# Kernel tuning notes

Measured on AMD Instinct MI355X. Metric: run time of the kernel, lower is better.

## Reference

```python
import jax, jax.numpy as jnp
import numpy as np

B, L, D = 32, 256, 1024
ALIGN = 1024
FF = 2048
NUM_CLASSES = 3


def setup_inputs() -> dict:
    key = jax.random.key(0)
    ks = jax.random.split(key, 10)
    u = lambda k, shape: jax.random.uniform(k, shape, jnp.float32, -1.0, 1.0)
    return {
        "premises": jax.random.normal(ks[0], (B, L, D), jnp.float32),
        "hypotheses": jax.random.normal(ks[1], (B, L, D), jnp.float32),
        "W_F": u(ks[2], (D, ALIGN)),
        "W_G": u(ks[3], (2 * D, FF)),
        "W1": u(ks[4], (2 * FF, FF)) * 0.02,
        "b1": jnp.zeros((FF,), jnp.float32),
        "W2": u(ks[5], (FF, FF)) * 0.02,
        "b2": jnp.zeros((FF,), jnp.float32),
        "W3": u(ks[6], (FF, NUM_CLASSES)) * 0.02,
        "b3": jnp.zeros((NUM_CLASSES,), jnp.float32),
    }


def reference(premises, hypotheses, W_F, W_G, W1, b1, W2, b2, W3, b3):
    # ---- align: tanh-projected cross attention ----
    F_p = jnp.tanh(jnp.einsum("bpd,da->bpa", premises, W_F))      # [B,Lp,A]
    F_h = jnp.tanh(jnp.einsum("bhd,da->bha", hypotheses, W_F))    # [B,Lh,A]
    eijs = jnp.einsum("bpa,bha->bph", F_p, F_h)                   # [B,Lp,Lh]
    attn = jax.nn.softmax(eijs, axis=-1)                          # tf.nn.softmax: last axis
    betas = jnp.einsum("bph,bhd->bpd", attn, hypotheses)          # [B,Lp,D]
    alphas = jnp.einsum("bph,bpd->bhd", attn, premises)           # [B,Lh,D]

    # ---- compare (dropout is identity: p_keep = 1.0 at eval) ----
    V1 = jnp.tanh(jnp.concatenate([premises, betas], axis=2) @ W_G)    # [B,Lp,FF]
    V2 = jnp.tanh(jnp.concatenate([hypotheses, alphas], axis=2) @ W_G) # [B,Lh,FF]

    # ---- aggregate: sum-pool over sequence, concat ----
    agg = jnp.concatenate([V1.sum(axis=1), V2.sum(axis=1)], axis=1)    # [B,2*FF]

    # ---- classifier MLP ----
    a1 = jnp.tanh(agg @ W1 + b1)
    a2 = jnp.tanh(a1 @ W2 + b2)
    logits = a2 @ W3 + b3                                              # [B,3]
    return logits
```

## Files before the change

### kernel.cpp

```cpp
#include <hip/hip_runtime.h>
#include <hip/hip_bf16.h>
#include <stdint.h>


typedef __attribute__((ext_vector_type(8))) short    short8_t;
typedef __attribute__((ext_vector_type(4))) float    float4_t;
typedef __attribute__((ext_vector_type(8))) _Float16 half8_t;
typedef __attribute__((ext_vector_type(4))) _Float16 half4_t;
typedef __attribute__((ext_vector_type(2))) _Float16 half2_t;

#define DEVI static __device__ __forceinline__

DEVI short f2bf(float f) {
  union { float f; unsigned u; } v; v.f = f;
  unsigned r = v.u + 0x7fffu + ((v.u >> 16) & 1u);
  return (short)(r >> 16);
}
DEVI float bf2f(short s) {
  union { unsigned u; float f; } v;
  v.u = ((unsigned)(unsigned short)s) << 16;
  return v.f;
}
DEVI void split2(float x, short& hi, short& lo) {
  hi = f2bf(x);
  lo = f2bf(x - bf2f(hi));
}
DEVI float fast_tanh(float x) {
  float e = __expf(2.0f * x);
  return 1.0f - 2.0f / (e + 1.0f);
}
DEVI void gload16(const void* g, void* l) {
  __builtin_amdgcn_global_load_lds(
      (const __attribute__((address_space(1))) void*)g,
      (__attribute__((address_space(3))) void*)l, 16, 0, 0);
}

template <int DO_TANH, int OUT_MODE>
__global__ __launch_bounds__(256) void gemm_nt_split(
    const short* __restrict__ Ah, const short* __restrict__ Al, int lda, long sA,
    const short* __restrict__ Bh, const short* __restrict__ Bl, int ldb, long sB,
    void* __restrict__ Ch, void* __restrict__ Cl, int ldc, long sC,
    int M, int K, int kslices)
{
  __shared__ __align__(16) short Ash[128 * 32];
  __shared__ __align__(16) short Asl[128 * 32];
  __shared__ __align__(16) short Bsh[128 * 32];
  __shared__ __align__(16) short Bsl[128 * 32];

  const int z  = blockIdx.z;
  const int zb = z / kslices;
  const int Ksub = K / kslices;
  const int zk = z - zb * kslices;
  const int kbeg = zk * Ksub, kend = kbeg + Ksub;

  Ah += (size_t)zb * sA;  Al += (size_t)zb * sA;
  Bh += (size_t)zb * sB;  Bl += (size_t)zb * sB;

  const int row0 = blockIdx.x * 128;
  const int col0 = blockIdx.y * 128;

  const int t    = threadIdx.x;
  const int lane = t & 63;
  const int wave = t >> 6;
  const int wr = wave >> 1, wc = wave & 1;
  const int m15 = lane & 15, q = lane >> 4;

  const int schk = ((t & 3) ^ ((t >> 3) & 3)) * 8;
  const short* pAh = Ah + (size_t)(row0 + (t >> 2)) * lda + kbeg + schk;
  const short* pAl = Al + (size_t)(row0 + (t >> 2)) * lda + kbeg + schk;
  const short* pBh = Bh + (size_t)(col0 + (t >> 2)) * ldb + kbeg + schk;
  const short* pBl = Bl + (size_t)(col0 + (t >> 2)) * ldb + kbeg + schk;
  const size_t a64 = (size_t)64 * lda, b64 = (size_t)64 * ldb;
  short* lAh = &Ash[wave * 512];
  short* lAl = &Asl[wave * 512];
  short* lBh = &Bsh[wave * 512];
  short* lBl = &Bsl[wave * 512];

  const int fs2 = (q ^ ((m15 >> 1) & 3)) * 8;

  float4_t acc[4][4];
#pragma unroll
  for (int i = 0; i < 4; ++i)
#pragma unroll
    for (int j = 0; j < 4; ++j) acc[i][j] = (float4_t)0.0f;

  for (int k0 = kbeg; k0 < kend; k0 += 32) {
    gload16(pAh, lAh);  gload16(pAh + a64, lAh + 2048);
    gload16(pAl, lAl);  gload16(pAl + a64, lAl + 2048);
    gload16(pBh, lBh);  gload16(pBh + b64, lBh + 2048);
    gload16(pBl, lBl);  gload16(pBl + b64, lBl + 2048);
    pAh += 32; pAl += 32; pBh += 32; pBl += 32;
    __syncthreads();

    short8_t ah[4], al[4];
#pragma unroll
    for (int i = 0; i < 4; ++i) {
      const int ra = (wr * 64 + i * 16 + m15) * 32 + fs2;
      ah[i] = *(const short8_t*)&Ash[ra];
      al[i] = *(const short8_t*)&Asl[ra];
    }
#pragma unroll
    for (int j = 0; j < 4; ++j) {
      const int rb = (wc * 64 + j * 16 + m15) * 32 + fs2;
      short8_t bh = *(const short8_t*)&Bsh[rb];
      short8_t bl = *(const short8_t*)&Bsl[rb];
#pragma unroll
      for (int i = 0; i < 4; ++i) {
        acc[i][j] = __builtin_amdgcn_mfma_f32_16x16x32_bf16(ah[i], bh, acc[i][j], 0, 0, 0);
        acc[i][j] = __builtin_amdgcn_mfma_f32_16x16x32_bf16(ah[i], bl, acc[i][j], 0, 0, 0);
        acc[i][j] = __builtin_amdgcn_mfma_f32_16x16x32_bf16(al[i], bh, acc[i][j], 0, 0, 0);
      }
    }
    __syncthreads();
  }

  short* Chs = (short*)Ch + (size_t)zb * sC;
  short* Cls = (short*)Cl + (size_t)zb * sC;
  float* Cf  = (float*)Ch + (size_t)(OUT_MODE == 2 ? z : zb) * sC;
#pragma unroll
  for (int i = 0; i < 4; ++i) {
#pragma unroll
    for (int r = 0; r < 4; ++r) {
      int gm = row0 + wr * 64 + i * 16 + q * 4 + r;
      if (gm < M) {
#pragma unroll
        for (int j = 0; j < 4; ++j) {
          int gn = col0 + wc * 64 + j * 16 + m15;
          float v = acc[i][j][r];
          if (DO_TANH) v = fast_tanh(v);
          if (OUT_MODE == 2) {
            Cf[(size_t)gm * ldc + gn] = v;
          } else {
            short hi, lo; split2(v, hi, lo);
            Chs[(size_t)gm * ldc + gn] = hi;
            Cls[(size_t)gm * ldc + gn] = lo;
          }
        }
      }
    }
  }
}

__global__ __launch_bounds__(256) void gemm_f16(
    const _Float16* __restrict__ A, int lda, long sA,
    const _Float16* __restrict__ B, int ldb, long sB,
    _Float16* __restrict__ C, int ldc, long sC,
    int K, int bxor)
{
  __shared__ __align__(16) _Float16 As[2 * 128 * 32];
  __shared__ __align__(16) _Float16 Bs[2 * 128 * 32];

  const int z = blockIdx.z;
  A += (size_t)z * sA;
  B += (size_t)(z ^ bxor) * sB;

  const int row0 = blockIdx.x * 128;
  const int col0 = blockIdx.y * 128;
  const int t = threadIdx.x, lane = t & 63, wave = t >> 6;
  const int wr = wave >> 1, wc = wave & 1;
  const int m15 = lane & 15, q = lane >> 4;

  const int srow = wave * 32 + (lane >> 2);
  const int cg   = ((lane & 3) ^ ((lane >> 3) & 3)) * 8;
  const _Float16* gA0 = A + (size_t)(row0 + srow) * lda + cg;
  const _Float16* gA1 = gA0 + (size_t)16 * lda;
  const _Float16* gB0 = B + (size_t)(col0 + srow) * ldb + cg;
  const _Float16* gB1 = gB0 + (size_t)16 * ldb;
  const _Float16* gA0b = gA0 + 32;
  const _Float16* gA1b = gA1 + 32;
  const _Float16* gB0b = gB0 + 32;
  const _Float16* gB1b = gB1 + 32;
  _Float16* lA0  = &As[(wave * 32) * 32];
  _Float16* lA1  = &As[(wave * 32 + 16) * 32];
  _Float16* lB0  = &Bs[(wave * 32) * 32];
  _Float16* lB1  = &Bs[(wave * 32 + 16) * 32];
  _Float16* lA0b = lA0 + 4096;
  _Float16* lA1b = lA1 + 4096;
  _Float16* lB0b = lB0 + 4096;
  _Float16* lB1b = lB1 + 4096;

  const int fs = (q ^ ((m15 >> 1) & 3)) * 8;
  int aoff[4], boff[4];
#pragma unroll
  for (int i = 0; i < 4; ++i) {
    aoff[i] = (wr * 64 + i * 16 + m15) * 32 + fs;
    boff[i] = (wc * 64 + i * 16 + m15) * 32 + fs;
  }

  float4_t acc[4][4];
#pragma unroll
  for (int i = 0; i < 4; ++i)
#pragma unroll
    for (int j = 0; j < 4; ++j) acc[i][j] = (float4_t)0.0f;

  for (int k0 = 0; k0 < K; k0 += 64) {
    gload16(gA0, lA0);  gload16(gA1, lA1);
    gload16(gB0, lB0);  gload16(gB1, lB1);
    gload16(gA0b, lA0b); gload16(gA1b, lA1b);
    gload16(gB0b, lB0b); gload16(gB1b, lB1b);
    gA0 += 64; gA1 += 64; gB0 += 64; gB1 += 64;
    gA0b += 64; gA1b += 64; gB0b += 64; gB1b += 64;
    __syncthreads();

#pragma unroll
    for (int h = 0; h < 2; ++h) {
      half8_t af[4], bfr[4];
#pragma unroll
      for (int i = 0; i < 4; ++i) af[i]  = *(const half8_t*)&As[h * 4096 + aoff[i]];
#pragma unroll
      for (int j = 0; j < 4; ++j) bfr[j] = *(const half8_t*)&Bs[h * 4096 + boff[j]];
#pragma unroll
      for (int i = 0; i < 4; ++i)
#pragma unroll
        for (int j = 0; j < 4; ++j)
          acc[i][j] = __builtin_amdgcn_mfma_f32_16x16x32_f16(af[i], bfr[j], acc[i][j], 0, 0, 0);
    }
    __syncthreads();
  }

  {
    _Float16* Cp = C + (size_t)z * sC;
#pragma unroll
    for (int i = 0; i < 4; ++i)
#pragma unroll
      for (int r = 0; r < 4; ++r) {
        int gm = row0 + wr * 64 + i * 16 + q * 4 + r;
#pragma unroll
        for (int j = 0; j < 4; ++j) {
          int gn = col0 + wc * 64 + j * 16 + m15;
          Cp[(size_t)gm * ldc + gn] = (_Float16)acc[i][j][r];
        }
      }
  }
}

__global__ __launch_bounds__(512, 2) void gemm_f16_sum8(
    const _Float16* __restrict__ A, int lda,
    const _Float16* __restrict__ B, int ldb,
    int K, float* __restrict__ agg)
{
  __shared__ __align__(16) _Float16 LDS[4][2 * 256 * 32];

  const int row0 = blockIdx.x * 256;
  const int col0 = blockIdx.y * 256;
  const int tid  = threadIdx.x;
  const int lane = tid & 63, wave = tid >> 6;
  const int wr = wave >> 2, wc = wave & 3;
  const int m15 = lane & 15, q = lane >> 4;
  const int nt = K / 32;

  const int srow = wave * 32 + (lane >> 2);
  const int cg   = ((lane & 3) ^ ((lane >> 3) & 3)) * 8;
  const _Float16* gA = A + (size_t)(row0 + srow) * lda + cg;
  const _Float16* gB = B + (size_t)(col0 + srow) * ldb + cg;

  auto stageA = [&](int t) {
    const _Float16* g = gA + t * 32;
    _Float16* l = &LDS[t & 3][wave * 1024];
    gload16(g, l);
    gload16(g + (size_t)16 * lda, l + 512);
  };
  auto stageB = [&](int t) {
    const _Float16* g = gB + t * 32;
    _Float16* l = &LDS[t & 3][8192 + wave * 1024];
    gload16(g, l);
    gload16(g + (size_t)16 * ldb, l + 512);
  };

  const int xq = (q ^ ((m15 >> 1) & 3)) * 8;
  int aoff[8], boff[4];
#pragma unroll
  for (int i = 0; i < 8; ++i)
    aoff[i] = (wr * 128 + i * 16 + m15) * 32 + xq;
#pragma unroll
  for (int j = 0; j < 4; ++j)
    boff[j] = 8192 + (wc * 64 + j * 16 + m15) * 32 + xq;

  float4_t acc[8][4];
#pragma unroll
  for (int i = 0; i < 8; ++i)
#pragma unroll
    for (int j = 0; j < 4; ++j) acc[i][j] = (float4_t)0.0f;

  stageA(0); stageB(0);
  stageA(1); stageB(1);
  asm volatile("s_waitcnt vmcnt(4)");
  __builtin_amdgcn_s_barrier();

  for (int t = 0; t < nt; ++t) {
    const _Float16* buf = &LDS[t & 3][0];
    __builtin_amdgcn_sched_barrier(0);

    half8_t a0[4], a1[4], bb[4];
#pragma unroll
    for (int i = 0; i < 4; ++i) a0[i] = *(const half8_t*)&buf[aoff[i]];
#pragma unroll
    for (int j = 0; j < 4; ++j) bb[j] = *(const half8_t*)&buf[boff[j]];
#pragma unroll
    for (int i = 0; i < 4; ++i) a1[i] = *(const half8_t*)&buf[aoff[4 + i]];

    if (t + 2 < nt) { stageA(t + 2); stageB(t + 2); }

    __builtin_amdgcn_s_setprio(1);
#pragma unroll
    for (int i = 0; i < 4; ++i)
#pragma unroll
      for (int j = 0; j < 4; ++j)
        acc[i][j] = __builtin_amdgcn_mfma_f32_16x16x32_f16(a0[i], bb[j], acc[i][j], 0, 0, 0);
#pragma unroll
    for (int i = 0; i < 4; ++i)
#pragma unroll
      for (int j = 0; j < 4; ++j)
        acc[4 + i][j] = __builtin_amdgcn_mfma_f32_16x16x32_f16(a1[i], bb[j], acc[4 + i][j], 0, 0, 0);
    __builtin_amdgcn_s_setprio(0);

    __builtin_amdgcn_sched_barrier(0);
    if (t + 2 < nt) {
      asm volatile("s_waitcnt vmcnt(4)");
    } else if (t + 1 < nt) {
      asm volatile("s_waitcnt vmcnt(0)");
    }
    __builtin_amdgcn_s_barrier();
  }

  const int half_ = row0 >= 8192;
  const int b     = (row0 & 8191) >> 8;
#pragma unroll
  for (int j = 0; j < 4; ++j) {
    float s = 0.0f;
#pragma unroll
    for (int i = 0; i < 8; ++i)
#pragma unroll
      for (int r = 0; r < 4; ++r) s += fast_tanh(acc[i][j][r]);
    s += __shfl_xor(s, 16);
    s += __shfl_xor(s, 32);
    if (q == 0) {
      int col = col0 + wc * 64 + j * 16 + m15;
      atomicAdd(&agg[(size_t)b * 4096 + half_ * 2048 + col], s);
    }
  }
}

__global__ __launch_bounds__(256) void transpose_w(
    const float* __restrict__ WF, short* __restrict__ oh, short* __restrict__ ol,
    const float* __restrict__ WG, _Float16* __restrict__ og)
{
  __shared__ float tile[32][33];
  const int id = blockIdx.x;
  const int tx = threadIdx.x & 31, ty = threadIdx.x >> 5;
  if (id < 1024) {
    const int c0 = (id & 31) * 32, r0 = (id >> 5) * 32;
#pragma unroll
    for (int i = 0; i < 4; ++i) {
      int r = ty + i * 8;
      tile[r][tx] = WF[(size_t)(r0 + r) * 1024 + c0 + tx];
    }
    __syncthreads();
#pragma unroll
    for (int i = 0; i < 4; ++i) {
      int cc = ty + i * 8;
      float v = tile[tx][cc];
      short hi, lo; split2(v, hi, lo);
      size_t o = (size_t)(c0 + cc) * 1024 + r0 + tx;
      oh[o] = hi;
      ol[o] = lo;
    }
  } else {
    const int t2 = id - 1024;
    const int c0 = (t2 & 63) * 32, r0 = (t2 >> 6) * 32;
#pragma unroll
    for (int i = 0; i < 4; ++i) {
      int r = ty + i * 8;
      tile[r][tx] = WG[(size_t)(r0 + r) * 2048 + c0 + tx];
    }
    __syncthreads();
#pragma unroll
    for (int i = 0; i < 4; ++i) {
      int cc = ty + i * 8;
      og[(size_t)(c0 + cc) * 2048 + r0 + tx] = (_Float16)tile[tx][cc];
    }
  }
}

__global__ __launch_bounds__(256) void transpose_b2b(
    const short* __restrict__ in, short* __restrict__ out,
    int R, int C, long sIn, long sOut)
{
  __shared__ short tile[32][33];
  in  += (size_t)blockIdx.z * sIn;
  out += (size_t)blockIdx.z * sOut;
  const int tx = threadIdx.x & 31, ty = threadIdx.x >> 5;
  const int c0 = blockIdx.x * 32, r0 = blockIdx.y * 32;
#pragma unroll
  for (int i = 0; i < 4; ++i) {
    int r = ty + i * 8;
    tile[r][tx] = in[(size_t)(r0 + r) * C + c0 + tx];
  }
  __syncthreads();
#pragma unroll
  for (int i = 0; i < 4; ++i) {
    int cc = ty + i * 8;
    out[(size_t)(c0 + cc) * R + r0 + tx] = tile[tx][cc];
  }
}

__global__ __launch_bounds__(256) void conv_in_t(
    const float* __restrict__ P, const float* __restrict__ Hh,
    short* __restrict__ oh, short* __restrict__ ol,
    _Float16* __restrict__ cat, _Float16* __restrict__ phbt,
    float* __restrict__ agg)
{
  __shared__ __align__(16) float tile[64][68];
  const int zb   = blockIdx.z;
  const int half = zb >> 5, b = zb & 31;
  const int bid = (zb * 4 + blockIdx.y) * 16 + blockIdx.x;
  if (bid < 128) {
    float4_t zz = (float4_t)0.0f;
    *(float4_t*)&agg[(size_t)bid * 1024 + threadIdx.x * 4] = zz;
  }
  const float* in = (half ? Hh : P) + (size_t)b * 256 * 1024;
  const int c0 = blockIdx.x * 64;
  const int r0 = blockIdx.y * 64;
  const int t  = threadIdx.x;
  const int rl = t >> 4;
  const int c4 = (t & 15) * 4;
  const size_t rowbase = (size_t)half * 8192 + (size_t)b * 256;
#pragma unroll
  for (int i = 0; i < 4; ++i) {
    int r = rl + i * 16;
    float4 v = *(const float4*)&in[(size_t)(r0 + r) * 1024 + c0 + c4];
    *(float4*)&tile[r][c4] = v;
    short4 h, l;
    split2(v.x, h.x, l.x); split2(v.y, h.y, l.y);
    split2(v.z, h.z, l.z); split2(v.w, h.w, l.w);
    size_t o = (rowbase + r0 + r) * 1024 + c0 + c4;
    *(short4*)&oh[o] = h;
    *(short4*)&ol[o] = l;
    half4_t c16;
    c16.x = (_Float16)v.x; c16.y = (_Float16)v.y;
    c16.z = (_Float16)v.z; c16.w = (_Float16)v.w;
    *(half4_t*)&cat[(rowbase + r0 + r) * 2048 + c0 + c4] = c16;
  }
  __syncthreads();
  _Float16* op = phbt + (size_t)zb * 1024 * 256;
  const int tx = t & 31;
  const int w  = t >> 5;
#pragma unroll
  for (int i = 0; i < 8; ++i) {
    int cc = w + i * 8;
    half2_t p;
    p.x = (_Float16)tile[tx * 2][cc];
    p.y = (_Float16)tile[tx * 2 + 1][cc];
    *(half2_t*)&op[(size_t)(c0 + cc) * 256 + r0 + tx * 2] = p;
  }
}

__global__ __launch_bounds__(256) void softmax_rows(
    const float* __restrict__ e, _Float16* __restrict__ attn)
{
  const int row  = blockIdx.x * 4 + (threadIdx.x >> 6);
  const int lane = threadIdx.x & 63;
  const size_t base = ((size_t)(row >> 8) * 4) * 65536
                    + (size_t)(row & 255) * 256 + lane * 4;
  const float4 v0 = *(const float4*)&e[base];
  const float4 v1 = *(const float4*)&e[base + 65536];
  const float4 v2 = *(const float4*)&e[base + 2 * 65536];
  const float4 v3 = *(const float4*)&e[base + 3 * 65536];
  float4 v;
  v.x = (v0.x + v1.x) + (v2.x + v3.x);
  v.y = (v0.y + v1.y) + (v2.y + v3.y);
  v.z = (v0.z + v1.z) + (v2.z + v3.z);
  v.w = (v0.w + v1.w) + (v2.w + v3.w);
  float m = fmaxf(fmaxf(v.x, v.y), fmaxf(v.z, v.w));
#pragma unroll
  for (int off = 32; off; off >>= 1) m = fmaxf(m, __shfl_xor(m, off));
  float e0 = __expf(v.x - m), e1 = __expf(v.y - m);
  float e2 = __expf(v.z - m), e3 = __expf(v.w - m);
  float s = e0 + e1 + e2 + e3;
#pragma unroll
  for (int off = 32; off; off >>= 1) s += __shfl_xor(s, off);
  float inv = 1.0f / s;
  half4_t o;
  o.x = (_Float16)(e0 * inv); o.y = (_Float16)(e1 * inv);
  o.z = (_Float16)(e2 * inv); o.w = (_Float16)(e3 * inv);
  *(half4_t*)&attn[(size_t)row * 256 + lane * 4] = o;
}

__global__ __launch_bounds__(256) void skinny_gemm(
    const float* __restrict__ A, const float* __restrict__ B,
    float* __restrict__ outp, int N, int K)
{
  __shared__ float Asl[256][33];
  const int n0 = blockIdx.x * 64;
  const int k0 = blockIdx.y * 256;
  const int t  = threadIdx.x;
#pragma unroll
  for (int j = 0; j < 32; ++j) {
    Asl[t][j] = A[(size_t)j * K + k0 + t];
  }
  __syncthreads();
  const int l = t & 63, w = t >> 6;
  const int n = n0 + l;
  float acc[8] = {0.f, 0.f, 0.f, 0.f, 0.f, 0.f, 0.f, 0.f};
  const float* Bp = B + (size_t)k0 * N + n;
#pragma unroll 4
  for (int k = 0; k < 256; ++k) {
    float bv = Bp[(size_t)k * N];
#pragma unroll
    for (int m = 0; m < 8; ++m)
      acc[m] += Asl[k][w * 8 + m] * bv;
  }
  float* o = outp + (size_t)blockIdx.y * 32 * N;
#pragma unroll
  for (int m = 0; m < 8; ++m)
    o[(size_t)(w * 8 + m) * N + n] = acc[m];
}

__global__ __launch_bounds__(256) void bias_sum_tanh(
    const float* __restrict__ parts, int nslice,
    const float* __restrict__ bias, float* __restrict__ o, int n)
{
  int i = blockIdx.x * 256 + threadIdx.x;
  if (i < n) {
    float s = 0.0f;
    for (int sl = 0; sl < nslice; ++sl) s += parts[(size_t)sl * n + i];
    o[i] = fast_tanh(s + bias[i & 2047]);
  }
}

__global__ __launch_bounds__(256) void logits2(
    const float* __restrict__ c2parts, const float* __restrict__ b2,
    const float* __restrict__ W3, const float* __restrict__ b3,
    float* __restrict__ out)
{
  const int b = blockIdx.x, t = threadIdx.x;
  float p0 = 0.f, p1 = 0.f, p2 = 0.f;
  for (int k = t; k < 2048; k += 256) {
    float c = 0.0f;
#pragma unroll
    for (int sl = 0; sl < 8; ++sl) c += c2parts[(size_t)sl * 65536 + b * 2048 + k];
    float a = fast_tanh(c + b2[k]);
    p0 += a * W3[k * 3 + 0];
    p1 += a * W3[k * 3 + 1];
    p2 += a * W3[k * 3 + 2];
  }
#pragma unroll
  for (int off = 32; off; off >>= 1) {
    p0 += __shfl_xor(p0, off);
    p1 += __shfl_xor(p1, off);
    p2 += __shfl_xor(p2, off);
  }
  __shared__ float red[4][3];
  if ((t & 63) == 0) {
    red[t >> 6][0] = p0; red[t >> 6][1] = p1; red[t >> 6][2] = p2;
  }
  __syncthreads();
  if (t < 3) out[b * 3 + t] = b3[t] + red[0][t] + red[1][t] + red[2][t] + red[3][t];
}

extern "C" void kernel_launch(void* const* d_in, const int* in_sizes, int n_in,
                              void* d_out, int out_size, void* d_ws, size_t ws_size,
                              hipStream_t stream) {
  (void)in_sizes; (void)n_in; (void)out_size; (void)ws_size;
  const float* P   = (const float*)d_in[0];
  const float* H   = (const float*)d_in[1];
  const float* W_F = (const float*)d_in[2];
  const float* W_G = (const float*)d_in[3];
  const float* W1  = (const float*)d_in[4];
  const float* b1  = (const float*)d_in[5];
  const float* W2  = (const float*)d_in[6];
  const float* b2  = (const float*)d_in[7];
  const float* W3  = (const float*)d_in[8];
  const float* b3  = (const float*)d_in[9];
  float* out = (float*)d_out;

  char* wsp = (char*)d_ws;
  auto alloc = [&](size_t bytes) {
    char* p = wsp;
    wsp += (bytes + 255) & ~(size_t)255;
    return p;
  };
  short*    Pp_h  = (short*)alloc(16384ull * 1024 * 2);
  short*    Pp_l  = (short*)alloc(16384ull * 1024 * 2);
  _Float16* Cat16 = (_Float16*)alloc(16384ull * 2048 * 2);
  short*    Fbuf  = (short*)alloc(32ull * 1024 * 1024 * 2);
  _Float16* PHbT  = (_Float16*)alloc(64ull * 1024 * 256 * 2);
  short*    WFT_h = (short*)alloc(1024ull * 1024 * 2);
  short*    WFT_l = (short*)alloc(1024ull * 1024 * 2);
  _Float16* WGT16 = (_Float16*)alloc(2048ull * 2048 * 2);
  _Float16* attn  = (_Float16*)alloc(32ull * 256 * 256 * 2);
  _Float16* attnT = (_Float16*)alloc(32ull * 256 * 256 * 2);
  float*    agg   = (float*)alloc(32ull * 4096 * 4);
  float*    a1f   = (float*)alloc(32ull * 2048 * 4);

  short* F_h = Fbuf;
  short* F_l = Fbuf + 16384ull * 1024;
  float* eparts  = (float*)Pp_h;
  float* c1parts = (float*)Pp_l;
  float* c2parts = (float*)(Pp_l + 4ull * 1024 * 1024);

  conv_in_t<<<dim3(16, 4, 64), 256, 0, stream>>>(P, H, Pp_h, Pp_l, Cat16, PHbT, agg);
  transpose_w<<<5120, 256, 0, stream>>>(W_F, WFT_h, WFT_l, W_G, WGT16);

  gemm_nt_split<1, 1><<<dim3(128, 8, 1), 256, 0, stream>>>(
      Pp_h, Pp_l, 1024, 0, WFT_h, WFT_l, 1024, 0,
      F_h, F_l, 1024, 0, 16384, 1024, 1);

  gemm_nt_split<0, 2><<<dim3(2, 2, 128), 256, 0, stream>>>(
      F_h, F_l, 1024, 256 * 1024,
      F_h + 8192ull * 1024, F_l + 8192ull * 1024, 1024, 256 * 1024,
      eparts, nullptr, 256, 65536, 256, 1024, 4);

  softmax_rows<<<2048, 256, 0, stream>>>(eparts, attn);
  transpose_b2b<<<dim3(8, 8, 32), 256, 0, stream>>>(
      (const short*)attn, (short*)attnT, 256, 256, 65536, 65536);

  gemm_f16<<<dim3(2, 8, 64), 256, 0, stream>>>(
      attn, 256, 65536, PHbT, 256, 1024 * 256,
      Cat16 + 1024, 2048, 256 * 2048, 256, 32);

  gemm_f16_sum8<<<dim3(64, 8, 1), 512, 0, stream>>>(
      Cat16, 2048, WGT16, 2048, 2048, agg);

  skinny_gemm<<<dim3(32, 16), 256, 0, stream>>>(agg, W1, c1parts, 2048, 4096);
  bias_sum_tanh<<<256, 256, 0, stream>>>(c1parts, 16, b1, a1f, 32 * 2048);
  skinny_gemm<<<dim3(32, 8), 256, 0, stream>>>(a1f, W2, c2parts, 2048, 2048);
  logits2<<<32, 256, 0, stream>>>(c2parts, b2, W3, b3, out);
}
```

Measured before the change: 560.4 us.

## Add dedicated triple-buffered split-bf16 GEMM for tanh W_F projection

Replaces the generic split-bf16 NT GEMM for the F = tanh(X·W_F) projection with a specialised kernel. It uses 512-thread blocks, 128x256 tiles, a three-slot LDS ring filled by direct global-to-LDS loads two k-steps ahead, XOR-swizzled LDS addressing to avoid bank conflicts, and raised wave priority around the MFMA block. The goal is to hide global load latency and improve MFMA use in the largest GEMM. The cost is 144KB of LDS per block, which limits occupancy, and hard-coded sizes that tie the kernel to these shapes.

```diff
diff --git a/kernel.cpp b/kernel.cpp
--- a/kernel.cpp
+++ b/kernel.cpp
@@ -33,6 +33,121 @@
   __builtin_amdgcn_global_load_lds(
       (const __attribute__((address_space(1))) void*)g,
       (__attribute__((address_space(3))) void*)l, 16, 0, 0);
+}
+
+__global__ __launch_bounds__(512, 2) void gemm_split_f(
+    const short* __restrict__ Ah, const short* __restrict__ Al,
+    const short* __restrict__ Bh, const short* __restrict__ Bl,
+    short* __restrict__ Fh, short* __restrict__ Fl)
+{
+  __shared__ __align__(16) short LDS[3][24576];
+
+  const int id   = blockIdx.x;
+  const int row0 = (id >> 2) * 128;
+  const int col0 = (id & 3) * 256;
+  const int tid  = threadIdx.x;
+  const int lane = tid & 63, wave = tid >> 6;
+  const int wr = wave >> 2, wc = wave & 3;
+  const int m15 = lane & 15, q = lane >> 4;
+  const int nt = 1024 / 32;
+
+  const int cg = ((lane & 3) ^ ((lane >> 3) & 3)) * 8;
+  const short* gptr[6];
+  int ldsoff[6];
+#pragma unroll
+  for (int c = 0; c < 6; ++c) {
+    const int f0 = wave * 96 + c * 16;
+    const int fr = f0 + (lane >> 2);
+    const short* base;
+    size_t roff;
+    if (f0 < 128)      { base = Ah; roff = (size_t)(row0 + fr) * 1024; }
+    else if (f0 < 256) { base = Al; roff = (size_t)(row0 + fr - 128) * 1024; }
+    else if (f0 < 512) { base = Bh; roff = (size_t)(col0 + fr - 256) * 1024; }
+    else               { base = Bl; roff = (size_t)(col0 + fr - 512) * 1024; }
+    gptr[c]   = base + roff + cg;
+    ldsoff[c] = f0 * 32;
+  }
+  auto stage = [&](short* slotbase, int kt) {
+#pragma unroll
+    for (int c = 0; c < 6; ++c)
+      gload16(gptr[c] + kt * 32, slotbase + ldsoff[c]);
+  };
+
+  const int xq = (q ^ ((m15 >> 1) & 3)) * 8;
+  int arow[4], brow[4];
+#pragma unroll
+  for (int i = 0; i < 4; ++i) {
+    arow[i] = (wr * 64 + i * 16 + m15) * 32 + xq;
+    brow[i] = 8192 + (wc * 64 + i * 16 + m15) * 32 + xq;
+  }
+
+  float4_t acc[4][4];
+#pragma unroll
+  for (int i = 0; i < 4; ++i)
+#pragma unroll
+    for (int j = 0; j < 4; ++j) acc[i][j] = (float4_t)0.0f;
+
+  stage(&LDS[0][0], 0);
+  stage(&LDS[1][0], 1);
+  asm volatile("s_waitcnt vmcnt(6)");
+  __builtin_amdgcn_s_barrier();
+
+  int cur = 0, st2 = 2;
+  for (int t = 0; t < nt; ++t) {
+    short* buf = &LDS[cur][0];
+    __builtin_amdgcn_sched_barrier(0);
+
+    short8_t ah[4], al[4], bh[4], bl[4];
+#pragma unroll
+    for (int i = 0; i < 4; ++i) {
+      ah[i] = *(const short8_t*)&buf[arow[i]];
+      al[i] = *(const short8_t*)&buf[arow[i] + 4096];
+    }
+#pragma unroll
+    for (int j = 0; j < 4; ++j) {
+      bh[j] = *(const short8_t*)&buf[brow[j]];
+      bl[j] = *(const short8_t*)&buf[brow[j] + 8192];
+    }
+
+    if (t + 2 < nt) stage(&LDS[st2][0], t + 2);
+
+    __builtin_amdgcn_s_setprio(1);
+#pragma unroll
+    for (int i = 0; i < 4; ++i)
+#pragma unroll
+      for (int j = 0; j < 4; ++j) {
+        acc[i][j] = __builtin_amdgcn_mfma_f32_16x16x32_bf16(ah[i], bh[j], acc[i][j], 0, 0, 0);
+        acc[i][j] = __builtin_amdgcn_mfma_f32_16x16x32_bf16(ah[i], bl[j], acc[i][j], 0, 0, 0);
+        acc[i][j] = __builtin_amdgcn_mfma_f32_16x16x32_bf16(al[i], bh[j], acc[i][j], 0, 0, 0);
+      }
+    __builtin_amdgcn_s_setprio(0);
+
+    __builtin_amdgcn_sched_barrier(0);
+    if (t + 2 < nt) {
+      asm volatile("s_waitcnt vmcnt(6)");
+    } else if (t + 1 < nt) {
+      asm volatile("s_waitcnt vmcnt(0)");
+    }
+    __builtin_amdgcn_s_barrier();
+    cur = (cur == 2) ? 0 : cur + 1;
+    st2 = (st2 == 2) ? 0 : st2 + 1;
+  }
+
+#pragma unroll
+  for (int i = 0; i < 4; ++i) {
+#pragma unroll
+    for (int r = 0; r < 4; ++r) {
+      const int gm = row0 + wr * 64 + i * 16 + q * 4 + r;
+#pragma unroll
+      for (int j = 0; j < 4; ++j) {
+        const int gn = col0 + wc * 64 + j * 16 + m15;
+        float v = fast_tanh(acc[i][j][r]);
+        short hi, lo; split2(v, hi, lo);
+        Fh[(size_t)gm * 1024 + gn] = hi;
+        Fl[(size_t)gm * 1024 + gn] = lo;
+      }
+    }
+  }
 }
 
 template <int DO_TANH, int OUT_MODE>
@@ -602,9 +717,7 @@
   conv_in_t<<<dim3(16, 4, 64), 256, 0, stream>>>(P, H, Pp_h, Pp_l, Cat16, PHbT, agg);
   transpose_w<<<5120, 256, 0, stream>>>(W_F, WFT_h, WFT_l, W_G, WGT16);
 
-  gemm_nt_split<1, 1><<<dim3(128, 8, 1), 256, 0, stream>>>(
-      Pp_h, Pp_l, 1024, 0, WFT_h, WFT_l, 1024, 0,
-      F_h, F_l, 1024, 0, 16384, 1024, 1);
+  gemm_split_f<<<512, 512, 0, stream>>>(Pp_h, Pp_l, WFT_h, WFT_l, F_h, F_l);
 
   gemm_nt_split<0, 2><<<dim3(2, 2, 128), 256, 0, stream>>>(
       F_h, F_l, 1024, 256 * 1024,
```

After: 547.4 us. -2.3%, faster.
